# Kernel optimization log

Hardware: AMD Instinct MI355X
Metric: run time of the kernel (lower is better)

Reference implementation:

```python
import jax, jax.numpy as jnp
import numpy as np

N = 4096          # detections per frame
M = 8192          # memory entries (tracks + backdrops)
D = 256           # embed_dim (hardcoded in module)
NUM_CLASSES = 80
OBJ_THR = 0.3
INIT_THR = 0.7
MATCH_THR = 0.5
NMS_CONF_THR = 0.5
NMS_BACKDROP_IOU = 0.3
NMS_CLASS_IOU = 0.7
NEG = -1e30


def bbox_iou(a, b):
    # a: [Na,4], b: [Nb,4] in (x1,y1,x2,y2) -> [Na,Nb]
    area_a = jnp.clip(a[:, 2] - a[:, 0], 0) * jnp.clip(a[:, 3] - a[:, 1], 0)
    area_b = jnp.clip(b[:, 2] - b[:, 0], 0) * jnp.clip(b[:, 3] - b[:, 1], 0)
    lt = jnp.maximum(a[:, None, :2], b[None, :, :2])
    rb = jnp.minimum(a[:, None, 2:], b[None, :, 2:])
    wh = jnp.clip(rb - lt, 0)
    inter = wh[..., 0] * wh[..., 1]
    return inter / jnp.clip(area_a[:, None] + area_b[None, :] - inter, 1e-6)


def setup_inputs() -> dict:
    key = jax.random.key(0)
    ks = jax.random.split(key, 8)
    xy = jax.random.uniform(ks[0], (N, 2)) * 1024.0
    wh = jax.random.uniform(ks[1], (N, 2)) * 200.0 + 8.0
    detections = jnp.concatenate([xy, xy + wh], axis=1)
    detection_scores = jax.random.uniform(ks[2], (N,))
    detection_class_ids = jax.random.randint(ks[3], (N,), 0, NUM_CLASSES)
    embeddings = jax.random.normal(ks[4], (N, D))
    memo_embeds = jax.random.normal(ks[5], (M, D))
    memo_class_ids = jax.random.randint(ks[6], (M,), 0, NUM_CLASSES)
    memo_track_ids = jax.random.randint(ks[7], (M,), 0, 10000)
    # last quarter of memory entries are backdrops (track_id == -1)
    memo_track_ids = memo_track_ids.at[3 * M // 4:].set(-1)
    return dict(
        detections=detections,
        detection_scores=detection_scores,
        detection_class_ids=detection_class_ids,
        embeddings=embeddings,
        memo_embeds=memo_embeds,
        memo_class_ids=memo_class_ids,
        memo_track_ids=memo_track_ids,
        num_tracks=10000,
    )


def reference(detections, detection_scores, detection_class_ids, embeddings,
              memo_embeds, memo_class_ids, memo_track_ids, num_tracks):
    # ---- remove_duplicates: sort by score desc, dual-threshold greedy NMS ----
    order = jnp.argsort(-detection_scores)
    boxes = detections[order]
    scores = detection_scores[order]
    cls = detection_class_ids[order]
    emb = embeddings[order]

    ious = bbox_iou(boxes, boxes)  # [N,N]
    thr = jnp.where(scores < OBJ_THR, NMS_BACKDROP_IOU, NMS_CLASS_IOU)
    lower = jnp.tril(jnp.ones((N, N), bool), -1)  # j < i (strict)
    # valids[i] depends only on ious against ALL higher-score dets (as in source)
    valid = ~(((ious > thr[:, None]) & lower).any(axis=1))

    # ---- bi-directional softmax similarity ----
    feats = emb @ memo_embeds.T  # [N,M]
    feats_m = jnp.where(valid[:, None], feats, NEG)  # invalid dets excluded
    d2t = jax.nn.softmax(feats_m, axis=1)
    t2d = jax.nn.softmax(feats_m, axis=0)
    sims = 0.5 * (d2t + t2d)
    cat_same = (cls[:, None] == memo_class_ids[None, :]).astype(sims.dtype)
    sims = sims * cat_same * valid[:, None].astype(sims.dtype)

    # ---- greedy per-detection matching (sequential: matched cols zeroed) ----
    col_ids = jnp.arange(M)

    def body(taken, inp):
        row, score = inp
        row = jnp.where(taken, 0.0, row)
        ind = jnp.argmax(row)
        conf = row[ind]
        cur = memo_track_ids[ind]
        match = conf > MATCH_THR
        is_track = cur > -1
        strong = score > OBJ_THR
        assign = match & is_track & strong
        idv = jnp.where(
            assign, cur,
            jnp.where(match & (~is_track) & (conf > NMS_CONF_THR), -2, -1))
        taken = taken | ((col_ids == ind) & assign)
        return taken, idv

    _, ids = jax.lax.scan(body, jnp.zeros((M,), bool), (sims, scores))

    # ---- create new tracks for confident unmatched detections ----
    new = (ids == -1) & (scores > INIT_THR) & valid
    offs = jnp.cumsum(new.astype(jnp.int32)) - 1
    ids = jnp.where(new, jnp.int32(num_tracks) + offs, ids)

    # ---- un-permute back to original detection order ----
    ids_out = jnp.zeros((N,), ids.dtype).at[order].set(ids)
    valid_out = jnp.zeros((N,), bool).at[order].set(valid)
    return ids_out, valid_out, sims
```

## Files before the change

kernel.cpp:

```cpp
#include <hip/hip_runtime.h>

#define NDET 4096
#define NMEM 8192
#define DEMB 256
#define CAP  64

static __device__ __forceinline__ float sim_val(float f, float rm, float rs,
                                                float cm, float cs, bool same) {
  if (!same) return 0.0f;
  return 0.5f * (expf(f - rm) / rs + expf(f - cm) / cs);
}

__global__ __launch_bounds__(256) void k_sort(const float* __restrict__ scores,
                                              const int* __restrict__ cls,
                                              const float* __restrict__ det,
                                              int* order, float* sscore, int* scls,
                                              float* sboxes) {
  __shared__ float s[NDET];
  int tid = threadIdx.x;
  for (int i = tid; i < NDET; i += 256) s[i] = scores[i];
  __syncthreads();
  int i = blockIdx.x * 256 + tid;
  float si = s[i];
  int rank = 0;
  for (int j = 0; j < NDET; ++j) {
    float sj = s[j];
    rank += (sj > si) || (sj == si && j < i);
  }
  order[rank] = i;
  sscore[rank] = si;
  scls[rank] = cls[i];
  ((float4*)sboxes)[rank] = ((const float4*)det)[i];
}

__global__ __launch_bounds__(256) void k_gather(const float* __restrict__ emb,
                                                const int* __restrict__ order,
                                                float* A) {
  int idx = blockIdx.x * 256 + threadIdx.x;
  int r = idx >> 6, lane = idx & 63;
  int o = order[r];
  ((float4*)A)[(size_t)r * 64 + lane] = ((const float4*)emb)[(size_t)o * 64 + lane];
}

__global__ __launch_bounds__(256) void k_valid(const float* __restrict__ sbox,
                                               const float* __restrict__ sscore,
                                               int* svalid) {
  int i = blockIdx.x, tid = threadIdx.x;
  float4 bi = ((const float4*)sbox)[i];
  float thr = (sscore[i] < 0.3f) ? 0.3f : 0.7f;
  float ai = fmaxf(bi.z - bi.x, 0.f) * fmaxf(bi.w - bi.y, 0.f);
  __shared__ int flag;
  if (tid == 0) flag = 0;
  __syncthreads();
  int any = 0;
  for (int j = tid; j < i; j += 256) {
    float4 bj = ((const float4*)sbox)[j];
    float aj = fmaxf(bj.z - bj.x, 0.f) * fmaxf(bj.w - bj.y, 0.f);
    float lx = fmaxf(bi.x, bj.x), ly = fmaxf(bi.y, bj.y);
    float rx = fminf(bi.z, bj.z), ry = fminf(bi.w, bj.w);
    float w = fmaxf(rx - lx, 0.f), h = fmaxf(ry - ly, 0.f);
    float inter = w * h;
    float den = fmaxf(ai + aj - inter, 1e-6f);
    any |= ((inter / den) > thr);
  }
  if (any) atomicOr(&flag, 1);
  __syncthreads();
  if (tid == 0) svalid[i] = flag ? 0 : 1;
}

__global__ __launch_bounds__(256) void k_zero(int* __restrict__ ccnt) {
  ccnt[blockIdx.x * 256 + threadIdx.x] = 0;
}

__global__ __launch_bounds__(256) void k_gemm1(const float* __restrict__ A,
                                               const float* __restrict__ B,
                                               const int* __restrict__ svalid,
                                               float2* __restrict__ rowpart,
                                               float2* __restrict__ colpart,
                                               float* __restrict__ feats) {
  __shared__ float As[32][132];
  __shared__ float Bs[32][132];
  __shared__ float red[128][17];
  __shared__ float tmax[128];
  __shared__ unsigned char vrow[128];
  const int tid = threadIdx.x;
  const int tx = tid & 15, ty = tid >> 4;
  const int j0 = blockIdx.x * 128, i0 = blockIdx.y * 128;
  if (tid < 128) vrow[tid] = (unsigned char)svalid[i0 + tid];
  float acc[8][8];
#pragma unroll
  for (int u = 0; u < 8; ++u)
#pragma unroll
    for (int v = 0; v < 8; ++v) acc[u][v] = 0.f;

  for (int kt = 0; kt < DEMB / 32; ++kt) {
    const int k0 = kt * 32;
    float4 av[4], bv[4];
    int rr[4], cc[4];
#pragma unroll
    for (int e = 0; e < 4; ++e) {
      int f = e * 256 + tid;
      rr[e] = f >> 3;
      cc[e] = (f & 7) << 2;
      av[e] = *(const float4*)(A + (size_t)(i0 + rr[e]) * DEMB + k0 + cc[e]);
      bv[e] = *(const float4*)(B + (size_t)(j0 + rr[e]) * DEMB + k0 + cc[e]);
    }
    __syncthreads();
#pragma unroll
    for (int e = 0; e < 4; ++e) {
      As[cc[e] + 0][rr[e]] = av[e].x;
      As[cc[e] + 1][rr[e]] = av[e].y;
      As[cc[e] + 2][rr[e]] = av[e].z;
      As[cc[e] + 3][rr[e]] = av[e].w;
      Bs[cc[e] + 0][rr[e]] = bv[e].x;
      Bs[cc[e] + 1][rr[e]] = bv[e].y;
      Bs[cc[e] + 2][rr[e]] = bv[e].z;
      Bs[cc[e] + 3][rr[e]] = bv[e].w;
    }
    __syncthreads();
#pragma unroll
    for (int kk = 0; kk < 32; ++kk) {
      float4 a0 = *(const float4*)&As[kk][ty * 8];
      float4 a1 = *(const float4*)&As[kk][ty * 8 + 4];
      float4 b0 = *(const float4*)&Bs[kk][tx * 8];
      float4 b1 = *(const float4*)&Bs[kk][tx * 8 + 4];
      float a[8] = {a0.x, a0.y, a0.z, a0.w, a1.x, a1.y, a1.z, a1.w};
      float b[8] = {b0.x, b0.y, b0.z, b0.w, b1.x, b1.y, b1.z, b1.w};
#pragma unroll
      for (int u = 0; u < 8; ++u)
#pragma unroll
        for (int v = 0; v < 8; ++v) acc[u][v] = __builtin_fmaf(a[u], b[v], acc[u][v]);
    }
  }
#pragma unroll
  for (int u = 0; u < 8; ++u) {
    int row = i0 + ty * 8 + u;
    float4 o0 = {acc[u][0], acc[u][1], acc[u][2], acc[u][3]};
    float4 o1 = {acc[u][4], acc[u][5], acc[u][6], acc[u][7]};
    *(float4*)(feats + (size_t)row * NMEM + j0 + tx * 8) = o0;
    *(float4*)(feats + (size_t)row * NMEM + j0 + tx * 8 + 4) = o1;
  }
  __syncthreads();
#pragma unroll
  for (int u = 0; u < 8; ++u) {
    float m = acc[u][0];
#pragma unroll
    for (int v = 1; v < 8; ++v) m = fmaxf(m, acc[u][v]);
    red[ty * 8 + u][tx] = m;
  }
  __syncthreads();
  if (tid < 128) {
    float m = red[tid][0];
#pragma unroll
    for (int t = 1; t < 16; ++t) m = fmaxf(m, red[tid][t]);
    tmax[tid] = m;
  }
  __syncthreads();
#pragma unroll
  for (int u = 0; u < 8; ++u) {
    float m = tmax[ty * 8 + u], s = 0.f;
#pragma unroll
    for (int v = 0; v < 8; ++v) s += expf(acc[u][v] - m);
    red[ty * 8 + u][tx] = s;
  }
  __syncthreads();
  if (tid < 128) {
    float s = 0.f;
#pragma unroll
    for (int t = 0; t < 16; ++t) s += red[tid][t];
    rowpart[(size_t)(i0 + tid) * 64 + blockIdx.x] = make_float2(tmax[tid], s);
  }
  __syncthreads();
#pragma unroll
  for (int v = 0; v < 8; ++v) {
    float m = -INFINITY;
#pragma unroll
    for (int u = 0; u < 8; ++u)
      if (vrow[ty * 8 + u]) m = fmaxf(m, acc[u][v]);
    red[tx * 8 + v][ty] = m;
  }
  __syncthreads();
  if (tid < 128) {
    float m = red[tid][0];
#pragma unroll
    for (int t = 1; t < 16; ++t) m = fmaxf(m, red[tid][t]);
    tmax[tid] = m;
  }
  __syncthreads();
#pragma unroll
  for (int v = 0; v < 8; ++v) {
    float m = tmax[tx * 8 + v], s = 0.f;
    if (m > -INFINITY) {
#pragma unroll
      for (int u = 0; u < 8; ++u)
        if (vrow[ty * 8 + u]) s += expf(acc[u][v] - m);
    }
    red[tx * 8 + v][ty] = s;
  }
  __syncthreads();
  if (tid < 128) {
    float s = 0.f;
#pragma unroll
    for (int t = 0; t < 16; ++t) s += red[tid][t];
    colpart[(size_t)(j0 + tid) * 32 + blockIdx.y] = make_float2(tmax[tid], s);
  }
}

__global__ __launch_bounds__(256) void k_rowmerge(const float2* __restrict__ rowpart,
                                                  float* rmax, float* rsum) {
  int r = blockIdx.x * 256 + threadIdx.x;
  float M = -INFINITY;
  for (int c = 0; c < 64; ++c) M = fmaxf(M, rowpart[(size_t)r * 64 + c].x);
  float s = 0.f;
  for (int c = 0; c < 64; ++c) {
    float2 p = rowpart[(size_t)r * 64 + c];
    s += p.y * expf(p.x - M);
  }
  rmax[r] = M;
  rsum[r] = s;
}

__global__ __launch_bounds__(256) void k_colmerge(const float2* __restrict__ colpart,
                                                  float* cmax, float* csum) {
  int c = blockIdx.x * 256 + threadIdx.x;
  float M = -INFINITY;
  for (int b = 0; b < 32; ++b) {
    float2 p = colpart[(size_t)c * 32 + b];
    if (p.y > 0.f) M = fmaxf(M, p.x);
  }
  float s = 0.f;
  for (int b = 0; b < 32; ++b) {
    float2 p = colpart[(size_t)c * 32 + b];
    if (p.y > 0.f) s += p.y * expf(p.x - M);
  }
  cmax[c] = M;
  csum[c] = s;
}

__global__ __launch_bounds__(256) void k_transform(float* __restrict__ sims,
                                                   const float* __restrict__ rmax,
                                                   const float* __restrict__ rsum,
                                                   const float* __restrict__ cmax,
                                                   const float* __restrict__ csum,
                                                   const int* __restrict__ scls,
                                                   const int* __restrict__ mcls,
                                                   const int* __restrict__ svalid,
                                                   float* __restrict__ cval,
                                                   int* __restrict__ cidx,
                                                   int* __restrict__ ccnt) {
  const int r = blockIdx.x, tid = threadIdx.x;
  float* row = sims + (size_t)r * NMEM;
  if (!svalid[r]) {
    float4 z = {0.f, 0.f, 0.f, 0.f};
#pragma unroll
    for (int it = 0; it < 8; ++it) *(float4*)(row + it * 1024 + tid * 4) = z;
    return;
  }
  const float rm = rmax[r], rs = rsum[r];
  const int rc = scls[r];
#pragma unroll
  for (int it = 0; it < 8; ++it) {
    int j = it * 1024 + tid * 4;
    float4 f = *(const float4*)(row + j);
    float4 o;
    o.x = sim_val(f.x, rm, rs, cmax[j + 0], csum[j + 0], rc == mcls[j + 0]);
    o.y = sim_val(f.y, rm, rs, cmax[j + 1], csum[j + 1], rc == mcls[j + 1]);
    o.z = sim_val(f.z, rm, rs, cmax[j + 2], csum[j + 2], rc == mcls[j + 2]);
    o.w = sim_val(f.w, rm, rs, cmax[j + 3], csum[j + 3], rc == mcls[j + 3]);
    *(float4*)(row + j) = o;
    float vs[4] = {o.x, o.y, o.z, o.w};
#pragma unroll
    for (int q = 0; q < 4; ++q) {
      if (vs[q] > 0.5f) {
        int ps = atomicAdd(&ccnt[r], 1);
        if (ps < CAP) {
          cval[(size_t)r * CAP + ps] = vs[q];
          cidx[(size_t)r * CAP + ps] = j + q;
        }
      }
    }
  }
}

__global__ __launch_bounds__(256) void k_match(
    float* __restrict__ cval, int* __restrict__ cidx, const int* __restrict__ ccnt,
    const float* __restrict__ sscore, const int* __restrict__ svalid,
    const int* __restrict__ order, const int* __restrict__ mtrack,
    const int* __restrict__ ntptr, const float* __restrict__ sims,
    float* __restrict__ out) {
  const int tid = threadIdx.x;
  __shared__ float sc[NDET];
  __shared__ unsigned char vl[NDET];
  __shared__ unsigned short cnt_s[NDET];
  __shared__ int ids_s[NDET];
  __shared__ unsigned int taken[NMEM / 32];
  __shared__ unsigned short rlist[NDET];
  __shared__ int part[256];
  __shared__ int nR_s;
  __shared__ float rv[256];
  __shared__ int ri[256];

  for (int r = tid; r < NDET; r += 256) {
    sc[r] = sscore[r];
    vl[r] = (unsigned char)svalid[r];
    int c = ccnt[r];
    cnt_s[r] = (unsigned short)(c > 65535 ? 65535 : c);
    ids_s[r] = -1;
  }
  taken[tid] = 0u;
  __syncthreads();
  for (int r = tid; r < NDET; r += 256) {
    int n = cnt_s[r];
    if (n == 0 || n > CAP) continue;
    float* cv = cval + (size_t)r * CAP;
    int* ci = cidx + (size_t)r * CAP;
    for (int a = 1; a < n; ++a) {
      float v = cv[a];
      int id = ci[a];
      int b = a - 1;
      while (b >= 0 && (cv[b] < v || (cv[b] == v && ci[b] > id))) {
        cv[b + 1] = cv[b];
        ci[b + 1] = ci[b];
        --b;
      }
      cv[b + 1] = v;
      ci[b + 1] = id;
    }
  }
  __syncthreads();
  const int base = tid * 16;
  int cn = 0;
  for (int k = 0; k < 16; ++k) cn += (cnt_s[base + k] > 0);
  part[tid] = cn;
  __syncthreads();
  if (tid == 0) {
    int run = 0;
    for (int t = 0; t < 256; ++t) { int v = part[t]; part[t] = run; run += v; }
    nR_s = run;
  }
  __syncthreads();
  {
    int pos = part[tid];
    for (int k = 0; k < 16; ++k) {
      int r = base + k;
      if (cnt_s[r] > 0) rlist[pos++] = (unsigned short)r;
    }
  }
  __syncthreads();
  const int nR = nR_s;

  for (int t = 0; t < nR; ++t) {
    const int r = rlist[t];
    const int c = cnt_s[r];
    if (c <= CAP) {
      if (tid == 0) {
        float conf = 0.f;
        int ind = -1;
        for (int q = 0; q < c; ++q) {
          int j = cidx[(size_t)r * CAP + q];
          if (!((taken[j >> 5] >> (j & 31)) & 1u)) {
            conf = cval[(size_t)r * CAP + q];
            ind = j;
            break;
          }
        }
        if (ind >= 0 && conf > 0.5f) {
          int cur = mtrack[ind];
          if (cur > -1) {
            if (sc[r] > 0.3f) { ids_s[r] = cur; taken[ind >> 5] |= (1u << (ind & 31)); }
          } else ids_s[r] = -2;
        }
      }
      __syncthreads();
    } else {
      const float* srow = sims + (size_t)r * NMEM;
      float bv = -1.f;
      int bi = 1 << 30;
      for (int j = tid; j < NMEM; j += 256) {
        float v = ((taken[j >> 5] >> (j & 31)) & 1u) ? 0.f : srow[j];
        if (v > bv || (v == bv && j < bi)) { bv = v; bi = j; }
      }
      rv[tid] = bv;
      ri[tid] = bi;
      __syncthreads();
      for (int off = 128; off > 0; off >>= 1) {
        if (tid < off) {
          float v2 = rv[tid + off];
          int i2 = ri[tid + off];
          if (v2 > rv[tid] || (v2 == rv[tid] && i2 < ri[tid])) { rv[tid] = v2; ri[tid] = i2; }
        }
        __syncthreads();
      }
      if (tid == 0) {
        float conf = rv[0];
        int ind = ri[0];
        if (conf > 0.5f) {
          int cur = mtrack[ind];
          if (cur > -1) {
            if (sc[r] > 0.3f) { ids_s[r] = cur; taken[ind >> 5] |= (1u << (ind & 31)); }
          } else ids_s[r] = -2;
        }
      }
      __syncthreads();
    }
  }

  int cntNew = 0;
  for (int k = 0; k < 16; ++k) {
    int r = base + k;
    cntNew += (ids_s[r] == -1 && sc[r] > 0.7f && vl[r]);
  }
  part[tid] = cntNew;
  __syncthreads();
  if (tid == 0) {
    int run = 0;
    for (int t2 = 0; t2 < 256; ++t2) { int v = part[t2]; part[t2] = run; run += v; }
  }
  __syncthreads();
  const int nt = ntptr[0];
  int off2 = part[tid];
  for (int k = 0; k < 16; ++k) {
    int r = base + k;
    if (ids_s[r] == -1 && sc[r] > 0.7f && vl[r]) { ids_s[r] = nt + off2; off2++; }
  }
  __syncthreads();
  for (int r = tid; r < NDET; r += 256) {
    int o = order[r];
    out[o] = (float)ids_s[r];
    out[NDET + o] = vl[r] ? 1.0f : 0.0f;
  }
}

extern "C" void kernel_launch(void* const* d_in, const int* in_sizes, int n_in,
                              void* d_out, int out_size, void* d_ws, size_t ws_size,
                              hipStream_t stream) {
  const float* det = (const float*)d_in[0];
  const float* scores = (const float*)d_in[1];
  const int* cls = (const int*)d_in[2];
  const float* emb = (const float*)d_in[3];
  const float* memo = (const float*)d_in[4];
  const int* mcls = (const int*)d_in[5];
  const int* mtrack = (const int*)d_in[6];
  const int* ntptr = (const int*)d_in[7];
  float* out = (float*)d_out;
  float* feats = out + 2 * NDET;

  char* ws = (char*)d_ws;
  size_t o_A = 0;
  size_t o_order = o_A + (size_t)NDET * DEMB * 4;
  size_t o_sscore = o_order + NDET * 4;
  size_t o_scls = o_sscore + NDET * 4;
  size_t o_svalid = o_scls + NDET * 4;
  size_t o_sbox = o_svalid + NDET * 4;
  size_t o_rowpart = o_sbox + NDET * 16;
  size_t o_colpart = o_rowpart + (size_t)NDET * 64 * 8;
  size_t o_rmax = o_colpart + (size_t)NMEM * 32 * 8;
  size_t o_rsum = o_rmax + NDET * 4;
  size_t o_cmax = o_rsum + NDET * 4;
  size_t o_csum = o_cmax + NMEM * 4;
  size_t o_cval = o_csum + NMEM * 4;
  size_t o_cidx = o_cval + (size_t)NDET * CAP * 4;
  size_t o_ccnt = o_cidx + (size_t)NDET * CAP * 4;

  float* A = (float*)(ws + o_A);
  int* order = (int*)(ws + o_order);
  float* sscore = (float*)(ws + o_sscore);
  int* scls = (int*)(ws + o_scls);
  int* svalid = (int*)(ws + o_svalid);
  float* sbox = (float*)(ws + o_sbox);
  float2* rowpart = (float2*)(ws + o_rowpart);
  float2* colpart = (float2*)(ws + o_colpart);
  float* rmax = (float*)(ws + o_rmax);
  float* rsum = (float*)(ws + o_rsum);
  float* cmax = (float*)(ws + o_cmax);
  float* csum = (float*)(ws + o_csum);
  float* cval = (float*)(ws + o_cval);
  int* cidx = (int*)(ws + o_cidx);
  int* ccnt = (int*)(ws + o_ccnt);

  k_sort<<<NDET / 256, 256, 0, stream>>>(scores, cls, det, order, sscore, scls, sbox);
  k_gather<<<NDET * 64 / 256, 256, 0, stream>>>(emb, order, A);
  k_valid<<<NDET, 256, 0, stream>>>(sbox, sscore, svalid);
  k_zero<<<NDET / 256, 256, 0, stream>>>(ccnt);
  k_gemm1<<<dim3(NMEM / 128, NDET / 128), 256, 0, stream>>>(A, memo, svalid, rowpart,
                                                            colpart, feats);
  k_rowmerge<<<NDET / 256, 256, 0, stream>>>(rowpart, rmax, rsum);
  k_colmerge<<<NMEM / 256, 256, 0, stream>>>(colpart, cmax, csum);
  k_transform<<<NDET, 256, 0, stream>>>(feats, rmax, rsum, cmax, csum, scls, mcls,
                                        svalid, cval, cidx, ccnt);
  k_match<<<1, 256, 0, stream>>>(cval, cidx, ccnt, sscore, svalid, order, mtrack,
                                 ntptr, feats, out);
}
```

Measured before the change: 643.8 us.

## Stage match candidates in LDS, alias GEMM shared memory, vectorize transform loads

The k_zero launch is folded into k_sort. k_gemm1 aliases its reduction buffers onto the tile buffers and adds a min-blocks launch bound so more workgroups fit per CU. k_transform loads cmax/csum/mcls as float4/int4 instead of scalar reads. The single-block k_match drops the per-row insertion sort and instead scans each row's unsorted candidates for the best untaken one, and it caches candidates, track ids and flags in LDS. The matching loop no longer synchronizes between candidate rows. The risks are the larger LDS footprint of k_match, tighter register limits in the GEMM, and byte-sized counts that clamp at 255.

```diff
diff --git a/kernel.cpp b/kernel.cpp
--- a/kernel.cpp
+++ b/kernel.cpp
@@ -4,6 +4,7 @@
 #define NMEM 8192
 #define DEMB 256
 #define CAP  64
+#define POOL 6144
 
 static __device__ __forceinline__ float sim_val(float f, float rm, float rs,
                                                 float cm, float cs, bool same) {
@@ -15,12 +16,13 @@
                                               const int* __restrict__ cls,
                                               const float* __restrict__ det,
                                               int* order, float* sscore, int* scls,
-                                              float* sboxes) {
+                                              float* sboxes, int* ccnt) {
   __shared__ float s[NDET];
   int tid = threadIdx.x;
   for (int i = tid; i < NDET; i += 256) s[i] = scores[i];
   __syncthreads();
   int i = blockIdx.x * 256 + tid;
+  ccnt[i] = 0;
   float si = s[i];
   int rank = 0;
   for (int j = 0; j < NDET; ++j) {
@@ -68,20 +70,17 @@
   if (tid == 0) svalid[i] = flag ? 0 : 1;
 }
 
-__global__ __launch_bounds__(256) void k_zero(int* __restrict__ ccnt) {
-  ccnt[blockIdx.x * 256 + threadIdx.x] = 0;
-}
-
-__global__ __launch_bounds__(256) void k_gemm1(const float* __restrict__ A,
-                                               const float* __restrict__ B,
-                                               const int* __restrict__ svalid,
-                                               float2* __restrict__ rowpart,
-                                               float2* __restrict__ colpart,
-                                               float* __restrict__ feats) {
-  __shared__ float As[32][132];
-  __shared__ float Bs[32][132];
-  __shared__ float red[128][17];
-  __shared__ float tmax[128];
+__global__ __launch_bounds__(256, 4) void k_gemm1(const float* __restrict__ A,
+                                                  const float* __restrict__ B,
+                                                  const int* __restrict__ svalid,
+                                                  float2* __restrict__ rowpart,
+                                                  float2* __restrict__ colpart,
+                                                  float* __restrict__ feats) {
+  __shared__ float smraw[2 * 32 * 132];
+  float (*As)[132] = (float (*)[132])smraw;
+  float (*Bs)[132] = (float (*)[132])(smraw + 32 * 132);
+  float (*red)[17] = (float (*)[17])smraw;
+  float* tmax = smraw + 128 * 17;
   __shared__ unsigned char vrow[128];
   const int tid = threadIdx.x;
   const int tx = tid & 15, ty = tid >> 4;
@@ -262,11 +261,14 @@
   for (int it = 0; it < 8; ++it) {
     int j = it * 1024 + tid * 4;
     float4 f = *(const float4*)(row + j);
+    float4 cm4 = *(const float4*)(cmax + j);
+    float4 cs4 = *(const float4*)(csum + j);
+    int4 mc4 = *(const int4*)(mcls + j);
     float4 o;
-    o.x = sim_val(f.x, rm, rs, cmax[j + 0], csum[j + 0], rc == mcls[j + 0]);
-    o.y = sim_val(f.y, rm, rs, cmax[j + 1], csum[j + 1], rc == mcls[j + 1]);
-    o.z = sim_val(f.z, rm, rs, cmax[j + 2], csum[j + 2], rc == mcls[j + 2]);
-    o.w = sim_val(f.w, rm, rs, cmax[j + 3], csum[j + 3], rc == mcls[j + 3]);
+    o.x = sim_val(f.x, rm, rs, cm4.x, cs4.x, rc == mc4.x);
+    o.y = sim_val(f.y, rm, rs, cm4.y, cs4.y, rc == mc4.y);
+    o.z = sim_val(f.z, rm, rs, cm4.z, cs4.z, rc == mc4.z);
+    o.w = sim_val(f.w, rm, rs, cm4.w, cs4.w, rc == mc4.w);
     *(float4*)(row + j) = o;
     float vs[4] = {o.x, o.y, o.z, o.w};
 #pragma unroll
@@ -283,54 +285,45 @@
 }
 
 __global__ __launch_bounds__(256) void k_match(
-    float* __restrict__ cval, int* __restrict__ cidx, const int* __restrict__ ccnt,
-    const float* __restrict__ sscore, const int* __restrict__ svalid,
-    const int* __restrict__ order, const int* __restrict__ mtrack,
-    const int* __restrict__ ntptr, const float* __restrict__ sims,
-    float* __restrict__ out) {
+    const float* __restrict__ cval, const int* __restrict__ cidx,
+    const int* __restrict__ ccnt, const float* __restrict__ sscore,
+    const int* __restrict__ svalid, const int* __restrict__ order,
+    const int* __restrict__ mtrack, const int* __restrict__ ntptr,
+    const float* __restrict__ sims, float* __restrict__ out) {
   const int tid = threadIdx.x;
-  __shared__ float sc[NDET];
-  __shared__ unsigned char vl[NDET];
-  __shared__ unsigned short cnt_s[NDET];
+  __shared__ float pv[POOL];
+  __shared__ int mt[NMEM];
   __shared__ int ids_s[NDET];
   __shared__ unsigned int taken[NMEM / 32];
-  __shared__ unsigned short rlist[NDET];
   __shared__ int part[256];
-  __shared__ int nR_s;
   __shared__ float rv[256];
   __shared__ int ri[256];
+  __shared__ unsigned short pi[POOL];
+  __shared__ unsigned short rlist[NDET];
+  __shared__ unsigned short cstart[NDET];
+  __shared__ unsigned char flags[NDET];
+  __shared__ unsigned char cnt_s[NDET];
+  __shared__ int nR_s;
 
   for (int r = tid; r < NDET; r += 256) {
-    sc[r] = sscore[r];
-    vl[r] = (unsigned char)svalid[r];
+    float s = sscore[r];
     int c = ccnt[r];
-    cnt_s[r] = (unsigned short)(c > 65535 ? 65535 : c);
+    flags[r] = (unsigned char)((svalid[r] ? 1 : 0) | (s > 0.3f ? 2 : 0) |
+                               (s > 0.7f ? 4 : 0));
+    cnt_s[r] = (unsigned char)(c > 255 ? 255 : c);
     ids_s[r] = -1;
   }
+  for (int j = tid; j < NMEM; j += 256) mt[j] = mtrack[j];
   taken[tid] = 0u;
   __syncthreads();
-  for (int r = tid; r < NDET; r += 256) {
-    int n = cnt_s[r];
-    if (n == 0 || n > CAP) continue;
-    float* cv = cval + (size_t)r * CAP;
-    int* ci = cidx + (size_t)r * CAP;
-    for (int a = 1; a < n; ++a) {
-      float v = cv[a];
-      int id = ci[a];
-      int b = a - 1;
-      while (b >= 0 && (cv[b] < v || (cv[b] == v && ci[b] > id))) {
-        cv[b + 1] = cv[b];
-        ci[b + 1] = ci[b];
-        --b;
-      }
-      cv[b + 1] = v;
-      ci[b + 1] = id;
-    }
-  }
-  __syncthreads();
+
   const int base = tid * 16;
-  int cn = 0;
-  for (int k = 0; k < 16; ++k) cn += (cnt_s[base + k] > 0);
+  int cn = 0, pool_need = 0;
+  for (int k = 0; k < 16; ++k) {
+    int c = cnt_s[base + k];
+    cn += (c > 0);
+    pool_need += (c > 0 && c <= CAP) ? c : 0;
+  }
   part[tid] = cn;
   __syncthreads();
   if (tid == 0) {
@@ -341,9 +334,33 @@
   __syncthreads();
   {
     int pos = part[tid];
+    for (int k = 0; k < 16; ++k)
+      if (cnt_s[base + k] > 0) rlist[pos++] = (unsigned short)(base + k);
+  }
+  __syncthreads();
+  part[tid] = pool_need;
+  __syncthreads();
+  if (tid == 0) {
+    int run = 0;
+    for (int t = 0; t < 256; ++t) { int v = part[t]; part[t] = run; run += v; }
+  }
+  __syncthreads();
+  {
+    int off = part[tid];
     for (int k = 0; k < 16; ++k) {
       int r = base + k;
-      if (cnt_s[r] > 0) rlist[pos++] = (unsigned short)r;
+      int c = cnt_s[r];
+      if (c == 0) continue;
+      if (c <= CAP) {
+        if (off + c <= POOL) {
+          cstart[r] = (unsigned short)off;
+          for (int q = 0; q < c; ++q) {
+            pv[off + q] = cval[(size_t)r * CAP + q];
+            pi[off + q] = (unsigned short)cidx[(size_t)r * CAP + q];
+          }
+        } else cstart[r] = 0xFFFFu;
+        off += c;
+      } else cstart[r] = 0xFFFFu;
     }
   }
   __syncthreads();
@@ -354,34 +371,42 @@
     const int c = cnt_s[r];
     if (c <= CAP) {
       if (tid == 0) {
-        float conf = 0.f;
-        int ind = -1;
-        for (int q = 0; q < c; ++q) {
-          int j = cidx[(size_t)r * CAP + q];
-          if (!((taken[j >> 5] >> (j & 31)) & 1u)) {
-            conf = cval[(size_t)r * CAP + q];
-            ind = j;
-            break;
+        float bvv = 0.f;
+        int bii = -1;
+        const unsigned int st = cstart[r];
+        if (st != 0xFFFFu) {
+          for (int q = 0; q < c; ++q) {
+            int j = pi[st + q];
+            if ((taken[j >> 5] >> (j & 31)) & 1u) continue;
+            float v = pv[st + q];
+            if (bii < 0 || v > bvv || (v == bvv && j < bii)) { bvv = v; bii = j; }
+          }
+        } else {
+          for (int q = 0; q < c; ++q) {
+            int j = cidx[(size_t)r * CAP + q];
+            if ((taken[j >> 5] >> (j & 31)) & 1u) continue;
+            float v = cval[(size_t)r * CAP + q];
+            if (bii < 0 || v > bvv || (v == bvv && j < bii)) { bvv = v; bii = j; }
           }
         }
-        if (ind >= 0 && conf > 0.5f) {
-          int cur = mtrack[ind];
+        if (bii >= 0 && bvv > 0.5f) {
+          int cur = mt[bii];
           if (cur > -1) {
-            if (sc[r] > 0.3f) { ids_s[r] = cur; taken[ind >> 5] |= (1u << (ind & 31)); }
+            if (flags[r] & 2) { ids_s[r] = cur; taken[bii >> 5] |= 1u << (bii & 31); }
           } else ids_s[r] = -2;
         }
       }
+    } else {
       __syncthreads();
-    } else {
       const float* srow = sims + (size_t)r * NMEM;
-      float bv = -1.f;
-      int bi = 1 << 30;
+      float bvv = -1.f;
+      int bii = 1 << 30;
       for (int j = tid; j < NMEM; j += 256) {
         float v = ((taken[j >> 5] >> (j & 31)) & 1u) ? 0.f : srow[j];
-        if (v > bv || (v == bv && j < bi)) { bv = v; bi = j; }
+        if (v > bvv || (v == bvv && j < bii)) { bvv = v; bii = j; }
       }
-      rv[tid] = bv;
-      ri[tid] = bi;
+      rv[tid] = bvv;
+      ri[tid] = bii;
       __syncthreads();
       for (int off = 128; off > 0; off >>= 1) {
         if (tid < off) {
@@ -395,20 +420,21 @@
         float conf = rv[0];
         int ind = ri[0];
         if (conf > 0.5f) {
-          int cur = mtrack[ind];
+          int cur = mt[ind];
           if (cur > -1) {
-            if (sc[r] > 0.3f) { ids_s[r] = cur; taken[ind >> 5] |= (1u << (ind & 31)); }
+            if (flags[r] & 2) { ids_s[r] = cur; taken[ind >> 5] |= 1u << (ind & 31); }
           } else ids_s[r] = -2;
         }
       }
       __syncthreads();
     }
   }
+  __syncthreads();
 
   int cntNew = 0;
   for (int k = 0; k < 16; ++k) {
     int r = base + k;
-    cntNew += (ids_s[r] == -1 && sc[r] > 0.7f && vl[r]);
+    cntNew += (ids_s[r] == -1 && (flags[r] & 4) && (flags[r] & 1));
   }
   part[tid] = cntNew;
   __syncthreads();
@@ -421,13 +447,13 @@
   int off2 = part[tid];
   for (int k = 0; k < 16; ++k) {
     int r = base + k;
-    if (ids_s[r] == -1 && sc[r] > 0.7f && vl[r]) { ids_s[r] = nt + off2; off2++; }
+    if (ids_s[r] == -1 && (flags[r] & 4) && (flags[r] & 1)) ids_s[r] = nt + off2++;
   }
   __syncthreads();
   for (int r = tid; r < NDET; r += 256) {
     int o = order[r];
     out[o] = (float)ids_s[r];
-    out[NDET + o] = vl[r] ? 1.0f : 0.0f;
+    out[NDET + o] = (flags[r] & 1) ? 1.0f : 0.0f;
   }
 }
 
@@ -478,10 +504,10 @@
   int* cidx = (int*)(ws + o_cidx);
   int* ccnt = (int*)(ws + o_ccnt);
 
-  k_sort<<<NDET / 256, 256, 0, stream>>>(scores, cls, det, order, sscore, scls, sbox);
+  k_sort<<<NDET / 256, 256, 0, stream>>>(scores, cls, det, order, sscore, scls, sbox,
+                                         ccnt);
   k_gather<<<NDET * 64 / 256, 256, 0, stream>>>(emb, order, A);
   k_valid<<<NDET, 256, 0, stream>>>(sbox, sscore, svalid);
-  k_zero<<<NDET / 256, 256, 0, stream>>>(ccnt);
   k_gemm1<<<dim3(NMEM / 128, NDET / 128), 256, 0, stream>>>(A, memo, svalid, rowpart,
                                                             colpart, feats);
   k_rowmerge<<<NDET / 256, 256, 0, stream>>>(rowpart, rmax, rsum);
```

Measured after the change: 605.2 us. -6.0%, faster.
